# Kernel optimization log

Hardware: AMD Instinct MI355X
Metric: run time of the kernel (lower is better)

The kernel has to match this reference:

```python
import jax, jax.numpy as jnp
import numpy as np
import math

N, C, T, V = 8, 256, 128, 25
H, HC = 8, 32            # num_heads, head_channels
W, DIL = 3, 1            # window, dilation
O = 256                  # out_channels
PAD = (W + (W - 1) * (DIL - 1) - 1) // 2
B, L = N * T, W * V


def _ln(x, g, b):
    m = jnp.mean(x, -1, keepdims=True)
    v = jnp.var(x, -1, keepdims=True)
    return (x - m) * jax.lax.rsqrt(v + 1e-5) * g + b


def setup_inputs() -> dict:
    key = jax.random.key(0)
    ks = iter(jax.random.split(key, 40))
    def w(shape):
        return jax.random.normal(next(ks), shape, jnp.float32) * 0.02
    d = {"x": jax.random.normal(next(ks), (N, C, T, V), jnp.float32)}
    d.update(
        ln1_g=jnp.ones((C,)), ln1_b=jnp.zeros((C,)),
        Wq=w((C, C)), bq=jnp.zeros((C,)), Wqa=w((C, H)), bqa=jnp.zeros((H,)),
        Wk=w((C, C)), bk=jnp.zeros((C,)), Wka=w((C, H)), bka=jnp.zeros((H,)),
        Wv=w((C, C)), bv=jnp.zeros((C,)), Wt=w((C, C)), bt=jnp.zeros((C,)),
        Wp=w((C, C)), bp=jnp.zeros((C,)),
        ffn_g=jnp.ones((C,)), ffn_b=jnp.zeros((C,)),
        W1=w((C, C)), b1=jnp.zeros((C,)), W2=w((C, C)), b2=jnp.zeros((C,)),
        tn_g=jnp.ones((C,)), tn_b=jnp.zeros((C,)),
        c1_w=w((C, O)), c1_b=jnp.zeros((O,)),
        c2_w=w((W, O, O)), c2_b=jnp.zeros((O,)),
    )
    return d


def reference(x, ln1_g, ln1_b, Wq, bq, Wqa, bqa, Wk, bk, Wka, bka, Wv, bv,
              Wt, bt, Wp, bp, ffn_g, ffn_b, W1, b1, W2, b2, tn_g, tn_b,
              c1_w, c1_b, c2_w, c2_b):
    scale = 1.0 / math.sqrt(HC)
    # ---- Unfold over time: build window of frames around each t (nn.Unfold) ----
    xp = jnp.pad(x, ((0, 0), (0, 0), (PAD, PAD), (0, 0)))
    win = jnp.stack([jax.lax.dynamic_slice_in_dim(xp, k * DIL, T, 2) for k in range(W)], 2)  # (N,C,W,T,V)
    seq = win.transpose(0, 3, 2, 4, 1).reshape(B, L, C)  # (N*T, W*V, C)

    sep = lambda z: z.reshape(B, L, H, HC).transpose(0, 2, 1, 3)  # (B,H,L,HC)
    grp = lambda z: z.transpose(0, 2, 1, 3).reshape(B, -1, C)

    # ---- SpatioTemporalAttention (eval: dropouts off) ----
    nx = _ln(seq, ln1_g, ln1_b)
    q = nx @ Wq + bq                                            # (B,L,C)
    qw = jax.nn.softmax((q @ Wqa + bqa).transpose(0, 2, 1) * scale, axis=-1)  # (B,H,L)
    pq = jnp.einsum('bhl,bhlc->bhc', qw, sep(q)).reshape(B, 1, C)             # pooled query
    keys = nx @ Wk + bk
    kw = jax.nn.softmax(((keys * pq) @ Wka + bka).transpose(0, 2, 1) * scale, axis=-1)
    pk = jnp.einsum('bhl,bhlc->bhc', kw, sep(keys))             # pooled key (B,H,HC)
    vals = sep(nx @ Wv + bv)
    kv = grp(vals * pk[:, :, None, :]) @ Wt + bt                # (B,L,C)
    attn = (kv + q) @ Wp + bp                                   # residual-in-heads == plain add

    # ---- AttentionBranch residual + FFN ----
    att = attn + seq
    f = _ln(att, ffn_g, ffn_b)
    y = jax.nn.gelu(f @ W1 + b1, approximate=False) @ W2 + b2 + att  # (B,L,C)

    # ---- temporal branch: LN -> regroup frames -> 1x1 conv -> GELU -> (W,1) conv stride W ----
    t5 = _ln(y, tn_g, tn_b).reshape(N, T, W, V, C)
    h = jax.nn.gelu(t5 @ c1_w + c1_b, approximate=False)        # (N,T,W,V,O)
    out = jnp.einsum('ntwvi,wio->ntvo', h, c2_w) + c2_b         # stride==kernel conv == window contraction
    return out.transpose(0, 3, 1, 2)                            # (N,O,T,V)
```

## Files before the change

kernel.cpp:

```cpp
#include <hip/hip_runtime.h>


#define DI __device__ __forceinline__

constexpr int CC   = 256;
constexpr int CL   = 75;
constexpr int CV   = 25;
constexpr int CT   = 128;
constexpr int TP   = 130;
constexpr int MPAD = 8 * TP * CV;
constexpr int MBL  = 1024 * CL;
constexpr int MOUT = 8 * CT * CV;
constexpr float SM_SCALE = 0.17677669529663687f;

typedef __bf16 bf16x8 __attribute__((ext_vector_type(8)));
typedef float f32x4 __attribute__((ext_vector_type(4)));

DI float bf2f(unsigned short u) { return __uint_as_float(((unsigned)u) << 16); }
DI float bf2f_lo(unsigned u) { return __uint_as_float(u << 16); }
DI float bf2f_hi(unsigned u) { return __uint_as_float(u & 0xffff0000u); }
DI unsigned short f2bf(float f) {
  unsigned u = __float_as_uint(f);
  u += 0x7fffu + ((u >> 16) & 1u);
  return (unsigned short)(u >> 16);
}
DI unsigned packbf(float a, float b) {
  return (unsigned)f2bf(a) | ((unsigned)f2bf(b) << 16);
}
DI float geluf(float x) { return 0.5f * x * (1.f + erff(x * 0.70710678118654752440f)); }

DI void gll16(const unsigned short* g, unsigned short* l) {
  __builtin_amdgcn_global_load_lds(
      (const __attribute__((address_space(1))) unsigned int*)g,
      (__attribute__((address_space(3))) unsigned int*)l, 16, 0, 0);
}

DI int arow(int r) {
  int b = r / CL;
  int l = r - b * CL;
  int w = l / CV;
  int v = l - w * CV;
  int t = b & (CT - 1);
  int n = b >> 7;
  return (n * TP + t + w) * CV + v;
}

__global__ __launch_bounds__(256) void k_transpose(const float* __restrict__ x,
                                                   unsigned short* __restrict__ xtp) {
  __shared__ float tile[32][33];
  const int n = blockIdx.z;
  const int c0 = blockIdx.x * 32;
  const int tv0 = blockIdx.y * 32;
  const int tx = threadIdx.x & 31, ty = threadIdx.x >> 5;
#pragma unroll
  for (int j = 0; j < 32; j += 8) {
    tile[ty + j][tx] = x[((size_t)(n * CC + c0 + ty + j)) * 3200 + tv0 + tx];
  }
  __syncthreads();
#pragma unroll
  for (int j = 0; j < 32; j += 8) {
    int tv = tv0 + ty + j;
    int st = tv / CV, v = tv - st * CV;
    size_t row = ((size_t)n * TP + st + 1) * CV + v;
    xtp[row * CC + c0 + tx] = f2bf(tile[tx][ty + j]);
  }
}

__global__ __launch_bounds__(256) void k_zero_pad(unsigned short* __restrict__ xtp) {
  int i = blockIdx.x * 256 + threadIdx.x;
  int c = i & 255;
  int rid = i >> 8;
  int n = rid / 50;
  int rem = rid - n * 50;
  int side = rem / 25;
  int v = rem - side * 25;
  size_t row = ((size_t)n * TP + side * (TP - 1)) * CV + v;
  xtp[row * CC + c] = 0;
}

struct TJobs {
  const float* src[9];
  unsigned short* dst[9];
  int stride[9];
  int off[9];
};
__global__ __launch_bounds__(256) void k_wtrans(TJobs J) {
  __shared__ float tile[32][33];
  const int j = blockIdx.z;
  const float* src = J.src[j];
  unsigned short* dst = J.dst[j];
  const int stride = J.stride[j], off = J.off[j];
  const int k0 = blockIdx.x * 32, n0 = blockIdx.y * 32;
  const int tx = threadIdx.x & 31, ty = threadIdx.x >> 5;
#pragma unroll
  for (int jj = 0; jj < 32; jj += 8)
    tile[ty + jj][tx] = src[(size_t)(k0 + ty + jj) * 256 + n0 + tx];
  __syncthreads();
  if (stride > 0) {
#pragma unroll
    for (int jj = 0; jj < 32; jj += 8)
      dst[(size_t)(n0 + ty + jj) * stride + off + k0 + tx] = f2bf(tile[tx][ty + jj]);
  } else {
    const int k = k0 + tx;
#pragma unroll
    for (int jj = 0; jj < 32; jj += 8)
      dst[(size_t)(k >> 3) * 2048 + (size_t)(n0 + ty + jj) * 8 + (k & 7)] =
          f2bf(tile[tx][ty + jj]);
  }
}

__global__ __launch_bounds__(256) void k_wtwp(const float* __restrict__ Wt,
                                              const float* __restrict__ Wq,
                                              const float* __restrict__ Wp,
                                              unsigned short* __restrict__ fusedB,
                                              unsigned short* __restrict__ WqWpT) {
  __shared__ float wrow[256];
  const int k = blockIdx.x, n = threadIdx.x;
  const float* src = blockIdx.y ? Wq : Wt;
  unsigned short* dst = blockIdx.y ? WqWpT : fusedB;
  wrow[n] = src[(size_t)k * 256 + n];
  __syncthreads();
  float acc = 0.f;
  for (int j = 0; j < 256; ++j) acc = fmaf(wrow[j], Wp[(size_t)j * 256 + n], acc);
  dst[(size_t)n * 256 + k] = f2bf(acc);
}

__global__ __launch_bounds__(256) void k_bias2(const float* __restrict__ bt,
                                               const float* __restrict__ Wp,
                                               const float* __restrict__ bp,
                                               const float* __restrict__ bq,
                                               const float* __restrict__ bk,
                                               const float* __restrict__ bv,
                                               float* __restrict__ bias2,
                                               float* __restrict__ bias3) {
  const int n = threadIdx.x;
  float acc = bp[n];
  float accq = 0.f;
  for (int j = 0; j < 256; ++j) {
    const float w = Wp[(size_t)j * 256 + n];
    acc = fmaf(bt[j], w, acc);
    accq = fmaf(bq[j], w, accq);
  }
  bias2[n] = acc;
  bias3[n] = bq[n];
  bias3[256 + n] = bk[n];
  bias3[512 + n] = bv[n];
  bias3[768 + n] = accq;
}

__global__ __launch_bounds__(256) void k_ln4(const unsigned short* __restrict__ X,
                                             const float* __restrict__ g,
                                             const float* __restrict__ b,
                                             unsigned short* __restrict__ Y) {
  const int row = blockIdx.x * 4 + (threadIdx.x >> 6);
  const int lane = threadIdx.x & 63;
  const uint2 u = *(const uint2*)(X + (size_t)row * CC + lane * 4);
  const float x0 = bf2f_lo(u.x), x1 = bf2f_hi(u.x), x2 = bf2f_lo(u.y), x3 = bf2f_hi(u.y);
  float s = x0 + x1 + x2 + x3;
  float q = x0 * x0 + x1 * x1 + x2 * x2 + x3 * x3;
#pragma unroll
  for (int o = 32; o; o >>= 1) { s += __shfl_xor(s, o); q += __shfl_xor(q, o); }
  const float mean = s * (1.f / CC);
  const float var = q * (1.f / CC) - mean * mean;
  const float rs = rsqrtf(var + 1e-5f);
  const float4 g4 = *(const float4*)(g + lane * 4);
  const float4 b4 = *(const float4*)(b + lane * 4);
  uint2 o2;
  o2.x = packbf((x0 - mean) * rs * g4.x + b4.x, (x1 - mean) * rs * g4.y + b4.y);
  o2.y = packbf((x2 - mean) * rs * g4.z + b4.z, (x3 - mean) * rs * g4.w + b4.w);
  *(uint2*)(Y + (size_t)row * CC + lane * 4) = o2;
}

template <int AMODE, int EPI, int KD, bool MULTI>
__global__ __launch_bounds__(512) void k_mgemm(const unsigned short* __restrict__ A,
                                               const unsigned short* __restrict__ BwT,
                                               const float* __restrict__ bias,
                                               unsigned short* __restrict__ Cout,
                                               float* __restrict__ FOut,
                                               int M) {
  if constexpr (MULTI) {
    const int z = blockIdx.y;
    BwT += (size_t)z * (256 * 256);
    bias += z * 256;
    Cout += (size_t)z * MPAD * CC;
  }
  __shared__ unsigned short SH[20480];
  const int tid = threadIdx.x;
  const int lane = tid & 63;
  const int wid = tid >> 6;
  const int wm = wid >> 2, wn = wid & 3;
  const int r0 = blockIdx.x * 64;
  f32x4 acc[2][4] = {};

  const bool sa = tid < 256;
  const int rA = r0 + (tid >> 2);
  const int rAc = (rA < M) ? rA : (M - 1);
  const int segs = ((tid & 3) ^ ((tid >> 3) & 3)) * 8;
  int hrb = 0;
  if (sa && AMODE == 4 && rA < M) {
    const int nb = rA / 3200, rr = rA - nb * 3200;
    const int tq = rr / 25, vq = rr - tq * 25;
    hrb = (nb * CT + tq) * CL + vq;
  }

  auto loadA4 = [&](int k0) -> uint4 {
    uint4 u = make_uint4(0, 0, 0, 0);
    if (!(sa && rA < M)) return u;
    const int w = k0 >> 8;
    u = *(const uint4*)(A + (size_t)(hrb + w * CV) * CC + (k0 & 255) + segs);
    return u;
  };
  auto stageB = [&](int buf, int k0) {
    unsigned short* bs = SH + 4096 + buf * 8192;
#pragma unroll
    for (int pp = 0; pp < 2; ++pp) {
      const int s = tid + pp * 512;
      const int cs = ((s & 3) ^ ((s >> 3) & 3)) * 8;
      gll16(BwT + (size_t)(s >> 2) * KD + k0 + cs, bs + s * 8);
    }
  };
  auto stageAg = [&](int buf, int k0) {
    if (sa) gll16(A + (size_t)rAc * CC + k0 + segs, SH + buf * 2048 + tid * 8);
  };
  const int swl = ((lane & 15) >> 1) & 3;
  auto mfmaStep = [&](int cur) {
    const unsigned short* as = SH + cur * 2048;
    const unsigned short* bs = SH + 4096 + cur * 8192;
    bf16x8 af[2], bfr[4];
#pragma unroll
    for (int mi = 0; mi < 2; ++mi)
      af[mi] = *(const bf16x8*)(as + (wm * 32 + mi * 16 + (lane & 15)) * 32 +
                                (((lane >> 4) ^ swl) * 8));
#pragma unroll
    for (int ni = 0; ni < 4; ++ni)
      bfr[ni] = *(const bf16x8*)(bs + (wn * 64 + ni * 16 + (lane & 15)) * 32 +
                                 (((lane >> 4) ^ swl) * 8));
#pragma unroll
    for (int mi = 0; mi < 2; ++mi)
#pragma unroll
      for (int ni = 0; ni < 4; ++ni)
        acc[mi][ni] = __builtin_amdgcn_mfma_f32_16x16x32_bf16(af[mi], bfr[ni], acc[mi][ni], 0, 0, 0);
  };

  constexpr int NT = KD / 32;
  if constexpr (AMODE == 0) {
    asm volatile("s_waitcnt vmcnt(0)" ::: "memory");
    stageB(0, 0);
    stageAg(0, 0);
    for (int t = 0; t < NT; ++t) {
      const int cur = t & 1;
      const bool more = (t + 1 < NT);
      if (more) { stageB(cur ^ 1, (t + 1) * 32); stageAg(cur ^ 1, (t + 1) * 32); }
      if (wid < 4) {
        if (more) asm volatile("s_waitcnt vmcnt(3)" ::: "memory");
        else      asm volatile("s_waitcnt vmcnt(0)" ::: "memory");
      } else {
        if (more) asm volatile("s_waitcnt vmcnt(2)" ::: "memory");
        else      asm volatile("s_waitcnt vmcnt(0)" ::: "memory");
      }
      __builtin_amdgcn_s_barrier();
      asm volatile("" ::: "memory");
      mfmaStep(cur);
      asm volatile("s_waitcnt lgkmcnt(0)" ::: "memory");
      __builtin_amdgcn_s_barrier();
      asm volatile("" ::: "memory");
    }
    __syncthreads();
  } else {
    {
      const uint4 a0 = loadA4(0);
      stageB(0, 0);
      if (sa) *(uint4*)(SH + tid * 8) = a0;
    }
    for (int t = 0; t < NT; ++t) {
      const int cur = t & 1;
      const bool more = (t + 1 < NT);
      if (more) {
        const uint4 an = loadA4((t + 1) * 32);
        stageB(cur ^ 1, (t + 1) * 32);
        if (sa) *(uint4*)(SH + (cur ^ 1) * 2048 + tid * 8) = an;
      }
      asm volatile("s_waitcnt lgkmcnt(0)" ::: "memory");
      if (more) asm volatile("s_waitcnt vmcnt(2)" ::: "memory");
      else      asm volatile("s_waitcnt vmcnt(0)" ::: "memory");
      __builtin_amdgcn_s_barrier();
      asm volatile("" ::: "memory");
      mfmaStep(cur);
      asm volatile("s_waitcnt lgkmcnt(0)" ::: "memory");
      __builtin_amdgcn_s_barrier();
      asm volatile("" ::: "memory");
    }
    if constexpr (EPI == 0) __syncthreads();
  }

  const int ln15 = lane & 15, lq = lane >> 4;
  if constexpr (EPI == 4) {
#pragma unroll
    for (int mi = 0; mi < 2; ++mi) {
#pragma unroll
      for (int ni = 0; ni < 4; ++ni) {
        const int col = wn * 64 + ni * 16 + ln15;
        const float bcol = bias[col];
        const int rbase = r0 + wm * 32 + mi * 16 + lq * 4;
        const int nb = rbase / 3200, rr = rbase - nb * 3200;
        float4 v;
        v.x = acc[mi][ni][0] + bcol;
        v.y = acc[mi][ni][1] + bcol;
        v.z = acc[mi][ni][2] + bcol;
        v.w = acc[mi][ni][3] + bcol;
        *(float4*)(FOut + (size_t)nb * 819200 + (size_t)col * 3200 + rr) = v;
      }
    }
  } else {
    constexpr int LDC = 260;
#pragma unroll
    for (int mi = 0; mi < 2; ++mi) {
#pragma unroll
      for (int ni = 0; ni < 4; ++ni) {
        const int col = wn * 64 + ni * 16 + ln15;
        const float bcol = bias[col];
#pragma unroll
        for (int rg = 0; rg < 4; ++rg) {
          const int lrow = wm * 32 + mi * 16 + lq * 4 + rg;
          SH[lrow * LDC + col] = f2bf(acc[mi][ni][rg] + bcol);
        }
      }
    }
    __syncthreads();
#pragma unroll
    for (int i = 0; i < 4; ++i) {
      const int idx = tid + i * 512;
      const int row = idx >> 5, ch = idx & 31;
      const int gr = r0 + row;
      if (gr < M)
        *(uint4*)(Cout + (size_t)gr * CC + ch * 8) = *(const uint4*)&SH[row * LDC + ch * 8];
    }
  }
}

__global__ __launch_bounds__(512, 4) void k_chain(
    const unsigned short* __restrict__ VP, const float* __restrict__ PK,
    const unsigned short* __restrict__ XTP, const unsigned short* __restrict__ QWPP,
    const unsigned short* __restrict__ fusedB, const float* __restrict__ bias2,
    const unsigned short* __restrict__ W1F, const float* __restrict__ b1,
    const unsigned short* __restrict__ W2F, const float* __restrict__ b2,
    const float* __restrict__ ffn_g, const float* __restrict__ ffn_b,
    const unsigned short* __restrict__ c1wF, const float* __restrict__ c1b,
    const float* __restrict__ tn_g, const float* __restrict__ tn_b,
    unsigned short* __restrict__ Hout) {
  constexpr int LDC = 264;
  __shared__ unsigned short SH[16896 + 4096 + 16384];
  unsigned short* ACT = SH;
  unsigned short* AS = SH + 16896;
  unsigned short* BS = SH + 16896 + 4096;
  const int tid = threadIdx.x;
  const int lane = tid & 63, wid = tid >> 6;
  const int wm = wid >> 2, wn = wid & 3;
  const int ln15 = lane & 15, lq = lane >> 4;
  const int swl = (ln15 >> 1) & 3;
  const int r0 = blockIdx.x * 64;

  const bool sa = tid < 256;
  const int rA = r0 + (tid >> 2);
  const int segs = ((tid & 3) ^ ((tid >> 3) & 3)) * 8;
  int ar = 0, bb = 0;
  if (sa) { ar = arow(rA); bb = rA / CL; }
  int xrow[8];
#pragma unroll
  for (int i = 0; i < 8; ++i)
    xrow[i] = arow(r0 + wm * 32 + (i >> 2) * 16 + lq * 4 + (i & 3));

  auto stageB = [&](const unsigned short* BwT, int KD, int buf, int k0) {
    unsigned short* bs = BS + buf * 8192;
#pragma unroll
    for (int pp = 0; pp < 2; ++pp) {
      const int s = tid + pp * 512;
      const int cs = ((s & 3) ^ ((s >> 3) & 3)) * 8;
      gll16(BwT + (size_t)(s >> 2) * KD + k0 + cs, bs + s * 8);
    }
  };
  auto loadA5 = [&](int k0) -> uint4 {
    uint4 u = make_uint4(0, 0, 0, 0);
    if (!sa) return u;
    const int kg = k0 + segs;
    const uint4 t4 = *(const uint4*)(VP + (size_t)ar * CC + kg);
    const float* sv = PK + bb * CC + kg;
    const float4 s0 = *(const float4*)sv;
    const float4 s1 = *(const float4*)(sv + 4);
    u.x = packbf(bf2f_lo(t4.x) * s0.x, bf2f_hi(t4.x) * s0.y);
    u.y = packbf(bf2f_lo(t4.y) * s0.z, bf2f_hi(t4.y) * s0.w);
    u.z = packbf(bf2f_lo(t4.z) * s1.x, bf2f_hi(t4.z) * s1.y);
    u.w = packbf(bf2f_lo(t4.w) * s1.z, bf2f_hi(t4.w) * s1.w);
    return u;
  };
  auto ln_inplace = [&](const float* g, const float* b) {
    const float4 g4 = *(const float4*)(g + lane * 4);
    const float4 b4 = *(const float4*)(b + lane * 4);
#pragma unroll
    for (int rr = 0; rr < 8; ++rr) {
      const int row = wid * 8 + rr;
      const uint2 u = *(const uint2*)(ACT + row * LDC + lane * 4);
      const float x0 = bf2f_lo(u.x), x1 = bf2f_hi(u.x);
      const float x2 = bf2f_lo(u.y), x3 = bf2f_hi(u.y);
      float s = x0 + x1 + x2 + x3;
      float q = x0 * x0 + x1 * x1 + x2 * x2 + x3 * x3;
#pragma unroll
      for (int o = 32; o; o >>= 1) { s += __shfl_xor(s, o); q += __shfl_xor(q, o); }
      const float mean = s * (1.f / CC);
      const float var = q * (1.f / CC) - mean * mean;
      const float rs = rsqrtf(var + 1e-5f);
      uint2 o2;
      o2.x = packbf((x0 - mean) * rs * g4.x + b4.x, (x1 - mean) * rs * g4.y + b4.y);
      o2.y = packbf((x2 - mean) * rs * g4.z + b4.z, (x3 - mean) * rs * g4.w + b4.w);
      *(uint2*)(ACT + row * LDC + lane * 4) = o2;
    }
  };
  auto gemmRB = [&](const unsigned short* WF, f32x4 (&a)[2][4]) {
    const unsigned short* bp = WF + (size_t)(wn * 64 + ln15) * 8 + lq * 2048;
    const unsigned short* ap = ACT + (wm * 32 + ln15) * LDC + lq * 8;
    bf16x8 bA[4], bB[4];
#pragma unroll
    for (int ni = 0; ni < 4; ++ni) bA[ni] = *(const bf16x8*)(bp + ni * 128);
#pragma unroll 1
    for (int tt = 0; tt < 4; ++tt) {
      const int t0 = tt * 2, t1 = t0 + 1;
#pragma unroll
      for (int ni = 0; ni < 4; ++ni)
        bB[ni] = *(const bf16x8*)(bp + ni * 128 + t1 * 8192);
      {
        bf16x8 af0[2];
#pragma unroll
        for (int mi = 0; mi < 2; ++mi)
          af0[mi] = *(const bf16x8*)(ap + mi * 16 * LDC + t0 * 32);
#pragma unroll
        for (int mi = 0; mi < 2; ++mi)
#pragma unroll
          for (int ni = 0; ni < 4; ++ni)
            a[mi][ni] = __builtin_amdgcn_mfma_f32_16x16x32_bf16(af0[mi], bA[ni], a[mi][ni], 0, 0, 0);
      }
      if (tt < 3) {
#pragma unroll
        for (int ni = 0; ni < 4; ++ni)
          bA[ni] = *(const bf16x8*)(bp + ni * 128 + (t0 + 2) * 8192);
      }
      {
        bf16x8 af1[2];
#pragma unroll
        for (int mi = 0; mi < 2; ++mi)
          af1[mi] = *(const bf16x8*)(ap + mi * 16 * LDC + t1 * 32);
#pragma unroll
        for (int mi = 0; mi < 2; ++mi)
#pragma unroll
          for (int ni = 0; ni < 4; ++ni)
            a[mi][ni] = __builtin_amdgcn_mfma_f32_16x16x32_bf16(af1[mi], bB[ni], a[mi][ni], 0, 0, 0);
      }
    }
  };

  f32x4 acc[2][4] = {};
  {
    const uint4 a0 = loadA5(0);
    stageB(fusedB, 256, 0, 0);
    if (sa) *(uint4*)(AS + tid * 8) = a0;
  }
  for (int t = 0; t < 8; ++t) {
    const int cur = t & 1;
    const bool more = (t + 1 < 8);
    if (more) {
      const uint4 an = loadA5((t + 1) * 32);
      stageB(fusedB, 256, cur ^ 1, (t + 1) * 32);
      if (sa) *(uint4*)(AS + (cur ^ 1) * 2048 + tid * 8) = an;
    }
    asm volatile("s_waitcnt lgkmcnt(0)" ::: "memory");
    if (more) asm volatile("s_waitcnt vmcnt(2)" ::: "memory");
    else      asm volatile("s_waitcnt vmcnt(0)" ::: "memory");
    __builtin_amdgcn_s_barrier();
    asm volatile("" ::: "memory");
    {
      bf16x8 af[2], bfr[4];
#pragma unroll
      for (int mi = 0; mi < 2; ++mi)
        af[mi] = *(const bf16x8*)(AS + cur * 2048 + (wm * 32 + mi * 16 + ln15) * 32 +
                                  ((lq ^ swl) * 8));
#pragma unroll
      for (int ni = 0; ni < 4; ++ni)
        bfr[ni] = *(const bf16x8*)(BS + cur * 8192 + (wn * 64 + ni * 16 + ln15) * 32 +
                                   ((lq ^ swl) * 8));
#pragma unroll
      for (int mi = 0; mi < 2; ++mi)
#pragma unroll
        for (int ni = 0; ni < 4; ++ni)
          acc[mi][ni] = __builtin_amdgcn_mfma_f32_16x16x32_bf16(af[mi], bfr[ni], acc[mi][ni], 0, 0, 0);
    }
    asm volatile("s_waitcnt lgkmcnt(0)" ::: "memory");
    __builtin_amdgcn_s_barrier();
    asm volatile("" ::: "memory");
  }
  f32x4 attres[2][4];
#pragma unroll
  for (int mi = 0; mi < 2; ++mi) {
#pragma unroll
    for (int ni = 0; ni < 4; ++ni) {
      const int col = wn * 64 + ni * 16 + ln15;
      const float bcol = bias2[col];
#pragma unroll
      for (int rg = 0; rg < 4; ++rg) {
        const size_t ro = (size_t)xrow[mi * 4 + rg] * CC + col;
        attres[mi][ni][rg] = acc[mi][ni][rg] + bcol + bf2f(QWPP[ro]) + bf2f(XTP[ro]);
        ACT[(wm * 32 + mi * 16 + lq * 4 + rg) * LDC + col] = f2bf(attres[mi][ni][rg]);
      }
    }
  }
  __syncthreads();
  ln_inplace(ffn_g, ffn_b);
  __syncthreads();

  f32x4 acc2[2][4] = {};
  gemmRB(W1F, acc2);
  __syncthreads();
#pragma unroll
  for (int mi = 0; mi < 2; ++mi)
#pragma unroll
    for (int ni = 0; ni < 4; ++ni) {
      const int col = wn * 64 + ni * 16 + ln15;
      const float bcol = b1[col];
#pragma unroll
      for (int rg = 0; rg < 4; ++rg)
        ACT[(wm * 32 + mi * 16 + lq * 4 + rg) * LDC + col] = f2bf(geluf(acc2[mi][ni][rg] + bcol));
    }
  __syncthreads();

  f32x4 acc3[2][4] = {};
  gemmRB(W2F, acc3);
  __syncthreads();
#pragma unroll
  for (int mi = 0; mi < 2; ++mi)
#pragma unroll
    for (int ni = 0; ni < 4; ++ni) {
      const int col = wn * 64 + ni * 16 + ln15;
      const float bcol = b2[col];
#pragma unroll
      for (int rg = 0; rg < 4; ++rg)
        ACT[(wm * 32 + mi * 16 + lq * 4 + rg) * LDC + col] =
            f2bf(acc3[mi][ni][rg] + bcol + attres[mi][ni][rg]);
    }
  __syncthreads();
  ln_inplace(tn_g, tn_b);
  __syncthreads();

  f32x4 acc4[2][4] = {};
  gemmRB(c1wF, acc4);
  __syncthreads();
#pragma unroll
  for (int mi = 0; mi < 2; ++mi)
#pragma unroll
    for (int ni = 0; ni < 4; ++ni) {
      const int col = wn * 64 + ni * 16 + ln15;
      const float bcol = c1b[col];
#pragma unroll
      for (int rg = 0; rg < 4; ++rg)
        ACT[(wm * 32 + mi * 16 + lq * 4 + rg) * LDC + col] = f2bf(geluf(acc4[mi][ni][rg] + bcol));
    }
  __syncthreads();
#pragma unroll
  for (int i = 0; i < 4; ++i) {
    const int idx = tid + i * 512;
    const int row = idx >> 5, ch = idx & 31;
    *(uint4*)(Hout + (size_t)(r0 + row) * CC + ch * 8) = *(const uint4*)&ACT[row * LDC + ch * 8];
  }
}

__global__ __launch_bounds__(256) void k_attpool2(
    const unsigned short* __restrict__ QPr, const unsigned short* __restrict__ KPr,
    const float* __restrict__ Wqa, const float* __restrict__ bqa,
    const float* __restrict__ Wka, const float* __restrict__ bka,
    float* __restrict__ PK) {
  __shared__ unsigned short rows[CL * CC];
  __shared__ float uu[8 * 258];
  __shared__ float lg[8 * 76];
  __shared__ float inv8[8];
  __shared__ float pq[256];
  __shared__ int arl[CL];
  const int b = blockIdx.x;
  const int t = threadIdx.x;

  if (t < CL) arl[t] = arow(b * CL + t);
  __syncthreads();

  auto dot_phase = [&](const float* b8) {
    const int c0 = (t & 63) * 4;
    for (int i = t; i < CL * 8; i += 256) {
      const int h = i / CL, l = i - h * CL;
      float acc = b8[h];
#pragma unroll 4
      for (int jj = 0; jj < CC; jj += 4) {
        const int c = (c0 + jj) & 255;
        const uint2 pr = *(const uint2*)&rows[l * CC + c];
        acc = fmaf(bf2f_lo(pr.x), uu[h * 258 + c], acc);
        acc = fmaf(bf2f_hi(pr.x), uu[h * 258 + c + 1], acc);
        acc = fmaf(bf2f_lo(pr.y), uu[h * 258 + c + 2], acc);
        acc = fmaf(bf2f_hi(pr.y), uu[h * 258 + c + 3], acc);
      }
      lg[h * 76 + l] = acc * SM_SCALE;
    }
  };
  auto softmax8 = [&]() {
    if (t < 8) {
      float m = -1e30f;
      for (int l = 0; l < CL; ++l) m = fmaxf(m, lg[t * 76 + l]);
      float s = 0.f;
      for (int l = 0; l < CL; ++l) {
        const float e = __expf(lg[t * 76 + l] - m);
        lg[t * 76 + l] = e;
        s += e;
      }
      inv8[t] = 1.f / s;
    }
  };

  for (int i = t; i < CL * 32; i += 256) {
    const int r = i >> 5, seg = i & 31;
    gll16(QPr + (size_t)arl[r] * CC + seg * 8, &rows[i * 8]);
  }
  for (int i = t; i < CC * 8; i += 256) {
    const int c = i >> 3, h = i & 7;
    uu[h * 258 + c] = Wqa[c * 8 + h];
  }
  __syncthreads();
  dot_phase(bqa);
  __syncthreads();
  softmax8();
  __syncthreads();
  {
    const int h = t >> 5;
    float acc = 0.f;
    for (int l = 0; l < CL; ++l) acc = fmaf(lg[h * 76 + l], bf2f(rows[l * CC + t]), acc);
    pq[t] = acc * inv8[h];
  }
  __syncthreads();

  for (int i = t; i < CL * 32; i += 256) {
    const int r = i >> 5, seg = i & 31;
    gll16(KPr + (size_t)arl[r] * CC + seg * 8, &rows[i * 8]);
  }
  for (int i = t; i < CC * 8; i += 256) {
    const int c = i >> 3, h = i & 7;
    uu[h * 258 + c] = pq[c] * Wka[c * 8 + h];
  }
  __syncthreads();
  dot_phase(bka);
  __syncthreads();
  softmax8();
  __syncthreads();
  {
    const int h = t >> 5;
    float acc = 0.f;
    for (int l = 0; l < CL; ++l) acc = fmaf(lg[h * 76 + l], bf2f(rows[l * CC + t]), acc);
    PK[(size_t)b * CC + t] = acc * inv8[h];
  }
}

extern "C" void kernel_launch(void* const* d_in, const int* in_sizes, int n_in,
                              void* d_out, int out_size, void* d_ws, size_t ws_size,
                              hipStream_t stream) {
  const float* x = (const float*)d_in[0];
  const float* ln1_g = (const float*)d_in[1];
  const float* ln1_b = (const float*)d_in[2];
  const float* Wq = (const float*)d_in[3];
  const float* bq = (const float*)d_in[4];
  const float* Wqa = (const float*)d_in[5];
  const float* bqa = (const float*)d_in[6];
  const float* Wk = (const float*)d_in[7];
  const float* bk = (const float*)d_in[8];
  const float* Wka = (const float*)d_in[9];
  const float* bka = (const float*)d_in[10];
  const float* Wv = (const float*)d_in[11];
  const float* bv = (const float*)d_in[12];
  const float* Wt = (const float*)d_in[13];
  const float* bt = (const float*)d_in[14];
  const float* Wp = (const float*)d_in[15];
  const float* bp = (const float*)d_in[16];
  const float* ffn_g = (const float*)d_in[17];
  const float* ffn_b = (const float*)d_in[18];
  const float* W1 = (const float*)d_in[19];
  const float* b1 = (const float*)d_in[20];
  const float* W2 = (const float*)d_in[21];
  const float* b2 = (const float*)d_in[22];
  const float* tn_g = (const float*)d_in[23];
  const float* tn_b = (const float*)d_in[24];
  const float* c1w = (const float*)d_in[25];
  const float* c1b = (const float*)d_in[26];
  const float* c2w = (const float*)d_in[27];
  const float* c2b = (const float*)d_in[28];
  float* out = (float*)d_out;

  char* wp = (char*)d_ws;
  auto alloc = [&](size_t bytes) -> char* {
    char* p = wp;
    wp += (bytes + 255) & ~(size_t)255;
    return p;
  };
  unsigned short* XTP = (unsigned short*)alloc((size_t)MPAD * CC * 2);
  unsigned short* LNXP = (unsigned short*)alloc((size_t)MPAD * CC * 2);
  unsigned short* QKVP = (unsigned short*)alloc((size_t)4 * MPAD * CC * 2);
  unsigned short* QP = QKVP;
  unsigned short* KP = QKVP + (size_t)MPAD * CC;
  unsigned short* VP = QKVP + (size_t)2 * MPAD * CC;
  unsigned short* QWPP = QKVP + (size_t)3 * MPAD * CC;
  unsigned short* Hb = (unsigned short*)alloc((size_t)MBL * CC * 2);
  float* PK = (float*)alloc((size_t)1024 * CC * 4);
  unsigned short* WqkvT = (unsigned short*)alloc((size_t)4 * 256 * 256 * 2);
  unsigned short* W1F = (unsigned short*)alloc(256 * 256 * 2);
  unsigned short* W2F = (unsigned short*)alloc(256 * 256 * 2);
  unsigned short* c1wF = (unsigned short*)alloc(256 * 256 * 2);
  unsigned short* c2wT = (unsigned short*)alloc(256 * 768 * 2);
  unsigned short* fusedB = (unsigned short*)alloc(256 * 256 * 2);
  float* bias2 = (float*)alloc(256 * 4);
  float* bias3 = (float*)alloc(1024 * 4);

  TJobs J;
  const float* srcs[9] = {Wq, Wk, Wv, W1, W2, c1w, c2w, c2w + 65536, c2w + 131072};
  unsigned short* dsts[9] = {WqkvT, WqkvT + 65536, WqkvT + 131072, W1F, W2F, c1wF,
                             c2wT, c2wT, c2wT};
  const int strides[9] = {256, 256, 256, 0, 0, 0, 768, 768, 768};
  const int offs[9] = {0, 0, 0, 0, 0, 0, 0, 256, 512};
  for (int i = 0; i < 9; ++i) {
    J.src[i] = srcs[i]; J.dst[i] = dsts[i]; J.stride[i] = strides[i]; J.off[i] = offs[i];
  }
  k_wtrans<<<dim3(8, 8, 9), 256, 0, stream>>>(J);
  k_wtwp<<<dim3(256, 2), 256, 0, stream>>>(Wt, Wq, Wp, fusedB, WqkvT + 3 * 65536);
  k_bias2<<<1, 256, 0, stream>>>(bt, Wp, bp, bq, bk, bv, bias2, bias3);

  k_transpose<<<dim3(8, 100, 8), 256, 0, stream>>>(x, XTP);
  k_zero_pad<<<400, 256, 0, stream>>>(XTP);
  k_ln4<<<MPAD / 4, 256, 0, stream>>>(XTP, ln1_g, ln1_b, LNXP);

  const int gP = (MPAD + 63) / 64;
  const int gO = MOUT / 64;
  k_mgemm<0, 0, 256, true><<<dim3(gP, 4), 512, 0, stream>>>(
      LNXP, WqkvT, bias3, QKVP, nullptr, MPAD);

  k_attpool2<<<1024, 256, 0, stream>>>(QP, KP, Wqa, bqa, Wka, bka, PK);

  k_chain<<<MBL / 64, 512, 0, stream>>>(VP, PK, XTP, QWPP, fusedB, bias2,
                                        W1F, b1, W2F, b2, ffn_g, ffn_b,
                                        c1wF, c1b, tn_g, tn_b, Hb);

  k_mgemm<4, 4, 768, false><<<gO, 512, 0, stream>>>(Hb, c2wT, c2b, nullptr, out, MOUT);
}
```

Before: 257.4 us.

## Load fusedB fragments directly from global in chain GEMM, drop LDS B staging

The first GEMM in k_chain now reads the fused Wt·Wp weight operand straight from global memory into registers in an MFMA-fragment-friendly layout. The weight-prep kernel writes that layout, and the double-buffered LDS staging of B is removed. This shrinks shared memory per block, and launch bounds are raised from 4 to 6 blocks per SM to use the freed occupancy. In exchange it relies on L2/cache hits for repeated weight reads and puts more register pressure on the tighter launch bound.

```diff
diff --git a/kernel.cpp b/kernel.cpp
--- a/kernel.cpp
+++ b/kernel.cpp
@@ -117,12 +117,14 @@
   __shared__ float wrow[256];
   const int k = blockIdx.x, n = threadIdx.x;
   const float* src = blockIdx.y ? Wq : Wt;
-  unsigned short* dst = blockIdx.y ? WqWpT : fusedB;
   wrow[n] = src[(size_t)k * 256 + n];
   __syncthreads();
   float acc = 0.f;
   for (int j = 0; j < 256; ++j) acc = fmaf(wrow[j], Wp[(size_t)j * 256 + n], acc);
-  dst[(size_t)n * 256 + k] = f2bf(acc);
+  if (blockIdx.y)
+    WqWpT[(size_t)n * 256 + k] = f2bf(acc);
+  else
+    fusedB[(size_t)(k >> 3) * 2048 + (size_t)n * 8 + (k & 7)] = f2bf(acc);
 }
 
 __global__ __launch_bounds__(256) void k_bias2(const float* __restrict__ bt,
@@ -338,7 +340,7 @@
   }
 }
 
-__global__ __launch_bounds__(512, 4) void k_chain(
+__global__ __launch_bounds__(512, 6) void k_chain(
     const unsigned short* __restrict__ VP, const float* __restrict__ PK,
     const unsigned short* __restrict__ XTP, const unsigned short* __restrict__ QWPP,
     const unsigned short* __restrict__ fusedB, const float* __restrict__ bias2,
@@ -349,10 +351,9 @@
     const float* __restrict__ tn_g, const float* __restrict__ tn_b,
     unsigned short* __restrict__ Hout) {
   constexpr int LDC = 264;
-  __shared__ unsigned short SH[16896 + 4096 + 16384];
+  __shared__ unsigned short SH[16896 + 4096];
   unsigned short* ACT = SH;
   unsigned short* AS = SH + 16896;
-  unsigned short* BS = SH + 16896 + 4096;
   const int tid = threadIdx.x;
   const int lane = tid & 63, wid = tid >> 6;
   const int wm = wid >> 2, wn = wid & 3;
@@ -370,15 +371,6 @@
   for (int i = 0; i < 8; ++i)
     xrow[i] = arow(r0 + wm * 32 + (i >> 2) * 16 + lq * 4 + (i & 3));
 
-  auto stageB = [&](const unsigned short* BwT, int KD, int buf, int k0) {
-    unsigned short* bs = BS + buf * 8192;
-#pragma unroll
-    for (int pp = 0; pp < 2; ++pp) {
-      const int s = tid + pp * 512;
-      const int cs = ((s & 3) ^ ((s >> 3) & 3)) * 8;
-      gll16(BwT + (size_t)(s >> 2) * KD + k0 + cs, bs + s * 8);
-    }
-  };
   auto loadA5 = [&](int k0) -> uint4 {
     uint4 u = make_uint4(0, 0, 0, 0);
     if (!sa) return u;
@@ -457,40 +449,62 @@
     }
   };
 
+  const unsigned short* g1bp = fusedB + (size_t)(wn * 64 + ln15) * 8 + lq * 2048;
   f32x4 acc[2][4] = {};
   {
     const uint4 a0 = loadA5(0);
-    stageB(fusedB, 256, 0, 0);
     if (sa) *(uint4*)(AS + tid * 8) = a0;
   }
-  for (int t = 0; t < 8; ++t) {
-    const int cur = t & 1;
-    const bool more = (t + 1 < 8);
-    if (more) {
-      const uint4 an = loadA5((t + 1) * 32);
-      stageB(fusedB, 256, cur ^ 1, (t + 1) * 32);
-      if (sa) *(uint4*)(AS + (cur ^ 1) * 2048 + tid * 8) = an;
+  bf16x8 bA[4], bB[4];
+#pragma unroll
+  for (int ni = 0; ni < 4; ++ni) bA[ni] = *(const bf16x8*)(g1bp + ni * 128);
+#pragma unroll 1
+  for (int tt = 0; tt < 4; ++tt) {
+    const int t1 = tt * 2 + 1;
+    {
+      const uint4 an = loadA5(t1 * 32);
+#pragma unroll
+      for (int ni = 0; ni < 4; ++ni)
+        bB[ni] = *(const bf16x8*)(g1bp + ni * 128 + t1 * 8192);
+      if (sa) *(uint4*)(AS + 2048 + tid * 8) = an;
     }
     asm volatile("s_waitcnt lgkmcnt(0)" ::: "memory");
-    if (more) asm volatile("s_waitcnt vmcnt(2)" ::: "memory");
-    else      asm volatile("s_waitcnt vmcnt(0)" ::: "memory");
     __builtin_amdgcn_s_barrier();
     asm volatile("" ::: "memory");
     {
-      bf16x8 af[2], bfr[4];
+      bf16x8 af[2];
 #pragma unroll
       for (int mi = 0; mi < 2; ++mi)
-        af[mi] = *(const bf16x8*)(AS + cur * 2048 + (wm * 32 + mi * 16 + ln15) * 32 +
-                                  ((lq ^ swl) * 8));
+        af[mi] = *(const bf16x8*)(AS + (wm * 32 + mi * 16 + ln15) * 32 + ((lq ^ swl) * 8));
+#pragma unroll
+      for (int mi = 0; mi < 2; ++mi)
+#pragma unroll
+        for (int ni = 0; ni < 4; ++ni)
+          acc[mi][ni] = __builtin_amdgcn_mfma_f32_16x16x32_bf16(af[mi], bA[ni], acc[mi][ni], 0, 0, 0);
+    }
+    asm volatile("s_waitcnt lgkmcnt(0)" ::: "memory");
+    __builtin_amdgcn_s_barrier();
+    asm volatile("" ::: "memory");
+    if (tt < 3) {
+      const uint4 an = loadA5((t1 + 1) * 32);
 #pragma unroll
       for (int ni = 0; ni < 4; ++ni)
-        bfr[ni] = *(const bf16x8*)(BS + cur * 8192 + (wn * 64 + ni * 16 + ln15) * 32 +
-                                   ((lq ^ swl) * 8));
+        bA[ni] = *(const bf16x8*)(g1bp + ni * 128 + (t1 + 1) * 8192);
+      if (sa) *(uint4*)(AS + tid * 8) = an;
+    }
+    asm volatile("s_waitcnt lgkmcnt(0)" ::: "memory");
+    __builtin_amdgcn_s_barrier();
+    asm volatile("" ::: "memory");
+    {
+      bf16x8 af[2];
 #pragma unroll
       for (int mi = 0; mi < 2; ++mi)
+        af[mi] = *(const bf16x8*)(AS + 2048 + (wm * 32 + mi * 16 + ln15) * 32 + ((lq ^ swl) * 8));
+#pragma unroll
+      for (int mi = 0; mi < 2; ++mi)
 #pragma unroll
         for (int ni = 0; ni < 4; ++ni)
-          acc[mi][ni] = __builtin_amdgcn_mfma_f32_16x16x32_bf16(af[mi], bfr[ni], acc[mi][ni], 0, 0, 0);
+          acc[mi][ni] = __builtin_amdgcn_mfma_f32_16x16x32_bf16(af[mi], bB[ni], acc[mi][ni], 0, 0, 0);
     }
     asm volatile("s_waitcnt lgkmcnt(0)" ::: "memory");
     __builtin_amdgcn_s_barrier();
```

New measurement: 262.3 us. Within noise of the previous version (+1.9%).
